# Kernel tuning notes

Measured on AMD Instinct MI355X. Metric: run time of the kernel, lower is better.

## Reference

```python
import jax, jax.numpy as jnp
import numpy as np

EPS = 1e-5
K = 3
N_TAP = K * K


def _bn(x, g, b, m, v):
    # eval-mode batchnorm over channel axis 1 of NCHW
    inv = g / jnp.sqrt(v + EPS)
    return x * inv[None, :, None, None] + (b - m * inv)[None, :, None, None]


def _silu(x):
    return x * jax.nn.sigmoid(x)


def _dcn(x, offset, mask, w, b, pad=1):
    """Modulated deformable conv (DCNv2), stride 1.
    x: [B,C,H,W], offset: [B,2n,H,W] ((dy,dx) per tap), mask: [B,n,H,W],
    w: [O,C,K,K], b: [O]."""
    B, C, H, W = x.shape
    O = w.shape[0]
    ky, kx = jnp.meshgrid(jnp.arange(K), jnp.arange(K), indexing='ij')
    ky = ky.reshape(N_TAP).astype(x.dtype)
    kx = kx.reshape(N_TAP).astype(x.dtype)
    off = offset.reshape(B, N_TAP, 2, H, W)
    base_y = jnp.arange(H, dtype=x.dtype)[None, None, :, None]
    base_x = jnp.arange(W, dtype=x.dtype)[None, None, None, :]
    # fractional sample positions [B,n,H,W]
    py = base_y - pad + ky[None, :, None, None] + off[:, :, 0]
    px = base_x - pad + kx[None, :, None, None] + off[:, :, 1]
    y0 = jnp.floor(py)
    x0 = jnp.floor(px)
    fy = py - y0
    fx = px - x0
    y0i = y0.astype(jnp.int32)
    x0i = x0.astype(jnp.int32)
    x_flat = x.reshape(B, C, 1, H * W)

    def corner(yi, xi, wgt):
        valid = (yi >= 0) & (yi < H) & (xi >= 0) & (xi < W)
        idx = (jnp.clip(yi, 0, H - 1) * W + jnp.clip(xi, 0, W - 1)).reshape(B, 1, N_TAP, H * W)
        v = jnp.take_along_axis(x_flat, idx, axis=-1)  # [B,C,n,HW]
        return v * (wgt * valid.astype(x.dtype)).reshape(B, 1, N_TAP, H * W)

    acc = corner(y0i, x0i, (1 - fy) * (1 - fx))
    acc = acc + corner(y0i, x0i + 1, (1 - fy) * fx)
    acc = acc + corner(y0i + 1, x0i, fy * (1 - fx))
    acc = acc + corner(y0i + 1, x0i + 1, fy * fx)
    val = acc.reshape(B, C, N_TAP, H, W) * mask[:, None]  # modulation
    out = jnp.einsum('bcnhw,ocn->bohw', val, w.reshape(O, C, N_TAP))
    return out + b[None, :, None, None]


def setup_inputs() -> dict:
    key = jax.random.key(0)
    ks = jax.random.split(key, 16)
    B, C1, H, W = 8, 256, 80, 80
    C2 = 256
    Ch = 128  # c_ = int(c2 * 0.5)
    d = {}
    d['x'] = jax.random.normal(ks[0], (B, C1, H, W), jnp.float32)
    # cv1: 1x1 conv (no bias) + BN
    d['cv1_w'] = jax.random.normal(ks[1], (Ch, C1), jnp.float32) * (1.0 / np.sqrt(C1))
    d['bn1_g'] = jax.random.uniform(ks[2], (Ch,), jnp.float32, 0.5, 1.5)
    d['bn1_b'] = jax.random.normal(ks[3], (Ch,), jnp.float32) * 0.1
    d['bn1_m'] = jax.random.normal(ks[4], (Ch,), jnp.float32) * 0.1
    d['bn1_v'] = jax.random.uniform(ks[5], (Ch,), jnp.float32, 0.5, 1.5)
    # offset/mask predictor 3x3 conv (small weights -> modest deformation)
    d['off_w'] = jax.random.normal(ks[6], (3 * N_TAP, Ch, K, K), jnp.float32) * 0.01
    d['off_b'] = jnp.zeros((3 * N_TAP,), jnp.float32)
    # dcn main weight/bias
    d['dcn_w'] = jax.random.normal(ks[7], (Ch, Ch, K, K), jnp.float32) * (1.0 / np.sqrt(Ch * N_TAP))
    d['dcn_b'] = jnp.zeros((Ch,), jnp.float32)
    d['bn2_g'] = jax.random.uniform(ks[8], (Ch,), jnp.float32, 0.5, 1.5)
    d['bn2_b'] = jax.random.normal(ks[9], (Ch,), jnp.float32) * 0.1
    d['bn2_m'] = jax.random.normal(ks[10], (Ch,), jnp.float32) * 0.1
    d['bn2_v'] = jax.random.uniform(ks[11], (Ch,), jnp.float32, 0.5, 1.5)
    # cv2: 1x1 conv (no bias) + BN
    d['cv2_w'] = jax.random.normal(ks[12], (C2, Ch), jnp.float32) * (1.0 / np.sqrt(Ch))
    d['bn3_g'] = jax.random.uniform(ks[13], (C2,), jnp.float32, 0.5, 1.5)
    d['bn3_b'] = jax.random.normal(ks[14], (C2,), jnp.float32) * 0.1
    d['bn3_m'] = jax.random.normal(ks[15], (C2,), jnp.float32) * 0.1
    d['bn3_v'] = jnp.ones((C2,), jnp.float32)
    return d


def reference(x, cv1_w, bn1_g, bn1_b, bn1_m, bn1_v,
              off_w, off_b, dcn_w, dcn_b, bn2_g, bn2_b, bn2_m, bn2_v,
              cv2_w, bn3_g, bn3_b, bn3_m, bn3_v):
    # cv1: 1x1 conv -> BN -> SiLU
    y = _silu(_bn(jnp.einsum('bchw,oc->bohw', x, cv1_w), bn1_g, bn1_b, bn1_m, bn1_v))
    # offset/mask predictor: 3x3 conv, pad 1
    raw = jax.lax.conv_general_dilated(
        y, off_w, window_strides=(1, 1), padding=((1, 1), (1, 1)),
        dimension_numbers=('NCHW', 'OIHW', 'NCHW')) + off_b[None, :, None, None]
    offset = raw[:, :2 * N_TAP]
    mask = jax.nn.sigmoid(raw[:, 2 * N_TAP:])
    # modulated deformable 3x3 conv -> BN -> SiLU
    y = _silu(_bn(_dcn(y, offset, mask, dcn_w, dcn_b), bn2_g, bn2_b, bn2_m, bn2_v))
    # cv2: 1x1 conv -> BN -> SiLU
    y = _silu(_bn(jnp.einsum('bchw,oc->bohw', y, cv2_w), bn3_g, bn3_b, bn3_m, bn3_v))
    return x + y  # shortcut (c1 == c2)
```

## Files before the change

kernel.cpp:

```cpp
#include <hip/hip_runtime.h>
#include <math.h>

#define HWSZ 6400
#define WIMG 80
#define HIMG 80
#define BEPS 1e-5f

typedef __attribute__((ext_vector_type(8))) short short8;
typedef __attribute__((ext_vector_type(4))) short s16x4;
typedef __attribute__((ext_vector_type(4))) float f32x4;

__device__ __forceinline__ unsigned short f2b(float f) {
    unsigned u = __builtin_bit_cast(unsigned, f);
    u += 0x7fffu + ((u >> 16) & 1u);
    return (unsigned short)(u >> 16);
}
__device__ __forceinline__ float b2f(unsigned short h) {
    unsigned u = ((unsigned)h) << 16;
    return __builtin_bit_cast(float, u);
}
__device__ __forceinline__ float silu_f(float t) { return t / (1.f + __expf(-t)); }

#define BPOS(sub, nt, n16, q) (((((sub)*4 + (nt))*16 + (n16))*40) + (q)*8)

__global__ __launch_bounds__(256) void k_prep(
    const float* __restrict__ cv1w, const float* __restrict__ g1, const float* __restrict__ b1,
    const float* __restrict__ m1, const float* __restrict__ v1,
    const float* __restrict__ offw, const float* __restrict__ offb,
    const float* __restrict__ dcnw, const float* __restrict__ dcnb,
    const float* __restrict__ g2, const float* __restrict__ b2,
    const float* __restrict__ m2, const float* __restrict__ v2,
    const float* __restrict__ cv2w, const float* __restrict__ g3, const float* __restrict__ b3,
    const float* __restrict__ m3, const float* __restrict__ v3,
    unsigned short* __restrict__ apk1, unsigned short* __restrict__ apko,
    unsigned short* __restrict__ apkd, unsigned short* __restrict__ apk2,
    float* __restrict__ bias1, float* __restrict__ biaso,
    float* __restrict__ bias2, float* __restrict__ bias3)
{
    int idx = blockIdx.x * 256 + threadIdx.x;
    if (idx < 32768) {
        int j = idx & 7, L = (idx >> 3) & 63, ks = (idx >> 9) & 7, mt = idx >> 12;
        int o = mt * 16 + (L & 15), k = ks * 32 + (L >> 4) * 8 + j;
        float inv = g1[o] * rsqrtf(v1[o] + BEPS);
        apk1[idx] = f2b(cv1w[o * 256 + k] * inv);
    } else if (idx < 69632) {
        int t = idx - 32768;
        int j = t & 7, L = (t >> 3) & 63;
        int mt = t / 18432, rem = t % 18432, ks = rem >> 9;
        int o = mt * 16 + (L & 15);
        int kp = ks * 32 + (L >> 4) * 8 + j;
        int n = kp >> 7, c = kp & 127;
        float wv = (o < 27) ? offw[(size_t)(o * 128 + c) * 9 + n] : 0.f;
        apko[t] = f2b(wv);
    } else if (idx < 217088) {
        int t = idx - 69632;
        int j = t & 7, L = (t >> 3) & 63;
        int mt = t / 18432, rem = t % 18432, ks = rem >> 9;
        int o = mt * 16 + (L & 15);
        int kp = ks * 32 + (L >> 4) * 8 + j;
        int n = kp >> 7, c = kp & 127;
        float inv = g2[o] * rsqrtf(v2[o] + BEPS);
        apkd[t] = f2b(dcnw[(size_t)(o * 128 + c) * 9 + n] * inv);
    } else if (idx < 249856) {
        int t = idx - 217088;
        int j = t & 7, L = (t >> 3) & 63, ks = (t >> 9) & 3, mt = t >> 11;
        int o = mt * 16 + (L & 15), k = ks * 32 + (L >> 4) * 8 + j;
        float inv = g3[o] * rsqrtf(v3[o] + BEPS);
        apk2[t] = f2b(cv2w[o * 128 + k] * inv);
    } else if (idx < 250395) {
        int t = idx - 249856;
        if (t < 128) { float inv = g1[t] * rsqrtf(v1[t] + BEPS); bias1[t] = b1[t] - m1[t] * inv; }
        else if (t < 155) { biaso[t - 128] = offb[t - 128]; }
        else if (t < 283) { int o = t - 155; float inv = g2[o] * rsqrtf(v2[o] + BEPS);
                            bias2[o] = dcnb[o] * inv + b2[o] - m2[o] * inv; }
        else { int o = t - 283; float inv = g3[o] * rsqrtf(v3[o] + BEPS); bias3[o] = b3[o] - m3[o] * inv; }
    }
}

__global__ __launch_bounds__(256) void k_cv1(
    const float* __restrict__ x, const unsigned short* __restrict__ apk1,
    const float* __restrict__ bias1, unsigned short* __restrict__ y1t)
{
    int blk = blockIdx.x;
    int b = blk & 7, pt = blk >> 3;
    int p0 = pt * 64;
    int tid = threadIdx.x;
    int lane = tid & 63, w = tid >> 6;
    int n16 = lane & 15, qd = lane >> 4;
    int px = p0 + w * 16 + n16;
    const float* xb = x + (size_t)b * 256 * HWSZ + px;
    f32x4 acc[8];
#pragma unroll
    for (int mt = 0; mt < 8; ++mt) acc[mt] = (f32x4){0.f, 0.f, 0.f, 0.f};
#pragma unroll 2
    for (int ks = 0; ks < 8; ++ks) {
        short8 bf;
#pragma unroll
        for (int j = 0; j < 8; ++j)
            bf[j] = (short)f2b(xb[(size_t)(ks * 32 + qd * 8 + j) * HWSZ]);
#pragma unroll
        for (int mt = 0; mt < 8; ++mt) {
            short8 af = *(const short8*)&apk1[(size_t)((mt * 8 + ks) * 64 + lane) * 8];
            acc[mt] = __builtin_amdgcn_mfma_f32_16x16x32_bf16(af, bf, acc[mt], 0, 0, 0);
        }
    }
    unsigned short* ytb = y1t + ((size_t)b * HWSZ + px) * 128;
#pragma unroll
    for (int mt = 0; mt < 8; ++mt) {
        int o0 = mt * 16 + qd * 4;
        s16x4 v;
#pragma unroll
        for (int r = 0; r < 4; ++r)
            v[r] = (short)f2b(silu_f(acc[mt][r] + bias1[o0 + r]));
        *(s16x4*)&ytb[o0] = v;
    }
}

__global__ __launch_bounds__(256) void k_off(
    const unsigned short* __restrict__ y1t, const unsigned short* __restrict__ apko,
    const float* __restrict__ biaso, float* __restrict__ raw)
{
    __shared__ __align__(16) unsigned short sV[10240];
    int blk = blockIdx.x;
    int b = blk & 7, pt = blk >> 3;
    int p0 = pt * 64;
    int tid = threadIdx.x;
    int lane = tid & 63, w = tid >> 6;
    int n16 = lane & 15, qd = lane >> 4;
    int pxl = tid >> 2, q = tid & 3;
    int p = p0 + pxl;
    int h = p / WIMG, wx = p % WIMG;
    const unsigned short* yb = y1t + (size_t)b * HWSZ * 128;
    f32x4 acc[2];
    acc[0] = (f32x4){0.f, 0.f, 0.f, 0.f};
    acc[1] = (f32x4){0.f, 0.f, 0.f, 0.f};
    const short8 zz = {0, 0, 0, 0, 0, 0, 0, 0};
    for (int n = 0; n < 9; ++n) {
        int hh = h - 1 + n / 3, ww = wx - 1 + n % 3;
        bool valid = ((unsigned)hh < HIMG) && ((unsigned)ww < WIMG);
        int spx = valid ? hh * WIMG + ww : 0;
        const unsigned short* ys = yb + (size_t)spx * 128 + q * 8;
#pragma unroll
        for (int sub = 0; sub < 4; ++sub) {
            short8 v = *(const short8*)&ys[sub * 32];
            if (!valid) v = zz;
            *(short8*)&sV[BPOS(sub, pxl >> 4, pxl & 15, q)] = v;
        }
        __syncthreads();
#pragma unroll
        for (int sub = 0; sub < 4; ++sub) {
            int ks = n * 4 + sub;
            short8 bf = *(const short8*)&sV[BPOS(sub, w, n16, qd)];
#pragma unroll
            for (int mi = 0; mi < 2; ++mi) {
                short8 af = *(const short8*)&apko[(size_t)((mi * 36 + ks) * 64 + lane) * 8];
                acc[mi] = __builtin_amdgcn_mfma_f32_16x16x32_bf16(af, bf, acc[mi], 0, 0, 0);
            }
        }
        __syncthreads();
    }
    float* rb = raw + (size_t)b * 27 * HWSZ + p0 + w * 16 + n16;
#pragma unroll
    for (int mi = 0; mi < 2; ++mi)
#pragma unroll
        for (int r = 0; r < 4; ++r) {
            int o = mi * 16 + qd * 4 + r;
            if (o < 27) {
                float t = acc[mi][r] + biaso[o];
                if (o >= 18) t = 1.f / (1.f + __expf(-t));
                rb[(size_t)o * HWSZ] = t;
            }
        }
}

__global__ __launch_bounds__(256) void k_dcn(
    const unsigned short* __restrict__ y1t, const float* __restrict__ raw,
    const unsigned short* __restrict__ apkd, const float* __restrict__ bias2,
    unsigned short* __restrict__ zt)
{
    __shared__ float swgt[4][9][64];
    __shared__ unsigned short sidx[4][9][64];
    __shared__ __align__(16) unsigned short sV[10240];
    int blk = blockIdx.x;
    int b = blk & 7, pt = blk >> 3;
    int p0 = pt * 64;
    int tid = threadIdx.x;

    for (int i = tid; i < 576; i += 256) {
        int n = i / 64, pp = i % 64;
        int p = p0 + pp;
        int h = p / WIMG, wx = p % WIMG;
        const float* rb = raw + (size_t)b * 27 * HWSZ + p;
        float dy = rb[(size_t)(2 * n) * HWSZ];
        float dx = rb[(size_t)(2 * n + 1) * HWSZ];
        float mk = rb[(size_t)(18 + n) * HWSZ];
        float py = (float)(h - 1 + n / 3) + dy;
        float px = (float)(wx - 1 + n % 3) + dx;
        float y0f = floorf(py), x0f = floorf(px);
        float fy = py - y0f, fx = px - x0f;
        int y0 = (int)y0f, x0 = (int)x0f;
#pragma unroll
        for (int k = 0; k < 4; ++k) {
            int yy = y0 + (k >> 1);
            int xx = x0 + (k & 1);
            bool valid = ((unsigned)yy < HIMG) && ((unsigned)xx < WIMG);
            float wk = ((k >> 1) ? fy : 1.f - fy) * ((k & 1) ? fx : 1.f - fx);
            wk = valid ? wk * mk : 0.f;
            int yc = min(max(yy, 0), HIMG - 1);
            int xc = min(max(xx, 0), WIMG - 1);
            sidx[k][n][pp] = (unsigned short)(yc * WIMG + xc);
            swgt[k][n][pp] = wk;
        }
    }
    __syncthreads();

    int lane = tid & 63, w = tid >> 6;
    int n16 = lane & 15, qd = lane >> 4;
    int pxl = tid >> 2, q = tid & 3;
    const unsigned short* yb = y1t + (size_t)b * HWSZ * 128;
    f32x4 acc[2][4];
#pragma unroll
    for (int mi = 0; mi < 2; ++mi)
#pragma unroll
        for (int nt = 0; nt < 4; ++nt) acc[mi][nt] = (f32x4){0.f, 0.f, 0.f, 0.f};

    for (int n = 0; n < 9; ++n) {
        float av[4][8];
#pragma unroll
        for (int sub = 0; sub < 4; ++sub)
#pragma unroll
            for (int j = 0; j < 8; ++j) av[sub][j] = 0.f;
#pragma unroll
        for (int k = 0; k < 4; ++k) {
            float wk = swgt[k][n][pxl];
            const unsigned short* ys = yb + (size_t)sidx[k][n][pxl] * 128 + q * 8;
#pragma unroll
            for (int sub = 0; sub < 4; ++sub) {
                short8 v = *(const short8*)&ys[sub * 32];
#pragma unroll
                for (int j = 0; j < 8; ++j)
                    av[sub][j] = fmaf(wk, b2f((unsigned short)v[j]), av[sub][j]);
            }
        }
#pragma unroll
        for (int sub = 0; sub < 4; ++sub) {
            short8 v;
#pragma unroll
            for (int j = 0; j < 8; ++j) v[j] = (short)f2b(av[sub][j]);
            *(short8*)&sV[BPOS(sub, pxl >> 4, pxl & 15, q)] = v;
        }
        __syncthreads();
#pragma unroll
        for (int sub = 0; sub < 4; ++sub) {
            int ks = n * 4 + sub;
            short8 bf[4];
#pragma unroll
            for (int nt = 0; nt < 4; ++nt)
                bf[nt] = *(const short8*)&sV[BPOS(sub, nt, n16, qd)];
#pragma unroll
            for (int mi = 0; mi < 2; ++mi) {
                short8 af = *(const short8*)&apkd[(size_t)(((2 * w + mi) * 36 + ks) * 64 + lane) * 8];
#pragma unroll
                for (int nt = 0; nt < 4; ++nt)
                    acc[mi][nt] = __builtin_amdgcn_mfma_f32_16x16x32_bf16(af, bf[nt], acc[mi][nt], 0, 0, 0);
            }
        }
        __syncthreads();
    }
    unsigned short* zb = zt + ((size_t)b * HWSZ + p0) * 128;
#pragma unroll
    for (int mi = 0; mi < 2; ++mi)
#pragma unroll
        for (int nt = 0; nt < 4; ++nt) {
            int o0 = (2 * w + mi) * 16 + qd * 4;
            int px = nt * 16 + n16;
            s16x4 v;
#pragma unroll
            for (int r = 0; r < 4; ++r)
                v[r] = (short)f2b(silu_f(acc[mi][nt][r] + bias2[o0 + r]));
            *(s16x4*)&zb[(size_t)px * 128 + o0] = v;
        }
}

__global__ __launch_bounds__(256) void k_cv2(
    const unsigned short* __restrict__ zt, const float* __restrict__ x,
    const unsigned short* __restrict__ apk2, const float* __restrict__ bias3,
    float* __restrict__ out)
{
    int blk = blockIdx.x;
    int b = blk & 7, pt = blk >> 3;
    int p0 = pt * 64;
    int tid = threadIdx.x;
    int lane = tid & 63, w = tid >> 6;
    int n16 = lane & 15, qd = lane >> 4;
    const unsigned short* zb = zt + ((size_t)b * HWSZ + p0) * 128;
    f32x4 acc[4][4];
#pragma unroll
    for (int mi = 0; mi < 4; ++mi)
#pragma unroll
        for (int nt = 0; nt < 4; ++nt) acc[mi][nt] = (f32x4){0.f, 0.f, 0.f, 0.f};
#pragma unroll
    for (int ks = 0; ks < 4; ++ks) {
        short8 bf[4];
#pragma unroll
        for (int nt = 0; nt < 4; ++nt)
            bf[nt] = *(const short8*)&zb[(size_t)(nt * 16 + n16) * 128 + ks * 32 + qd * 8];
#pragma unroll
        for (int mi = 0; mi < 4; ++mi) {
            int mt = w * 4 + mi;
            short8 af = *(const short8*)&apk2[(size_t)((mt * 4 + ks) * 64 + lane) * 8];
#pragma unroll
            for (int nt = 0; nt < 4; ++nt)
                acc[mi][nt] = __builtin_amdgcn_mfma_f32_16x16x32_bf16(af, bf[nt], acc[mi][nt], 0, 0, 0);
        }
    }
    const float* xb = x + (size_t)b * 256 * HWSZ;
    float* ob = out + (size_t)b * 256 * HWSZ;
#pragma unroll
    for (int mi = 0; mi < 4; ++mi)
#pragma unroll
        for (int nt = 0; nt < 4; ++nt)
#pragma unroll
            for (int r = 0; r < 4; ++r) {
                int o = w * 64 + mi * 16 + qd * 4 + r;
                size_t idx = (size_t)o * HWSZ + p0 + nt * 16 + n16;
                ob[idx] = xb[idx] + silu_f(acc[mi][nt][r] + bias3[o]);
            }
}

extern "C" void kernel_launch(void* const* d_in, const int* in_sizes, int n_in,
                              void* d_out, int out_size, void* d_ws, size_t ws_size,
                              hipStream_t stream) {
    const float* x     = (const float*)d_in[0];
    const float* cv1w  = (const float*)d_in[1];
    const float* bn1g  = (const float*)d_in[2];
    const float* bn1b  = (const float*)d_in[3];
    const float* bn1m  = (const float*)d_in[4];
    const float* bn1v  = (const float*)d_in[5];
    const float* offw  = (const float*)d_in[6];
    const float* offb  = (const float*)d_in[7];
    const float* dcnw  = (const float*)d_in[8];
    const float* dcnb  = (const float*)d_in[9];
    const float* bn2g  = (const float*)d_in[10];
    const float* bn2b  = (const float*)d_in[11];
    const float* bn2m  = (const float*)d_in[12];
    const float* bn2v  = (const float*)d_in[13];
    const float* cv2w  = (const float*)d_in[14];
    const float* bn3g  = (const float*)d_in[15];
    const float* bn3b  = (const float*)d_in[16];
    const float* bn3m  = (const float*)d_in[17];
    const float* bn3v  = (const float*)d_in[18];
    float* out = (float*)d_out;

    float* base = (float*)d_ws;
    unsigned short* y1t = (unsigned short*)base;
    float* raw   = base + 3276800;
    unsigned short* zt  = (unsigned short*)(base + 4659200);
    unsigned short* apk1 = (unsigned short*)(base + 7936000);
    unsigned short* apko = (unsigned short*)(base + 7952384);
    unsigned short* apkd = (unsigned short*)(base + 7970816);
    unsigned short* apk2 = (unsigned short*)(base + 8044544);
    float* bias1 = base + 8060928;
    float* biaso = base + 8061056;
    float* bias2 = base + 8061088;
    float* bias3 = base + 8061216;

    k_prep<<<979, 256, 0, stream>>>(cv1w, bn1g, bn1b, bn1m, bn1v,
                                    offw, offb, dcnw, dcnb,
                                    bn2g, bn2b, bn2m, bn2v,
                                    cv2w, bn3g, bn3b, bn3m, bn3v,
                                    apk1, apko, apkd, apk2,
                                    bias1, biaso, bias2, bias3);
    k_cv1<<<800, 256, 0, stream>>>(x, apk1, bias1, y1t);
    k_off<<<800, 256, 0, stream>>>(y1t, apko, biaso, raw);
    k_dcn<<<800, 256, 0, stream>>>(y1t, raw, apkd, bias2, zt);
    k_cv2<<<800, 256, 0, stream>>>(zt, x, apk2, bias3, out);
}
```

Measured before the change: 260.3 us.

## Vectorize epilogue stores, drop LDS staging in offset conv, pack bf16 conversions

```diff
diff --git a/kernel.cpp b/kernel.cpp
--- a/kernel.cpp
+++ b/kernel.cpp
@@ -9,11 +9,19 @@
 typedef __attribute__((ext_vector_type(8))) short short8;
 typedef __attribute__((ext_vector_type(4))) short s16x4;
 typedef __attribute__((ext_vector_type(4))) float f32x4;
+typedef __attribute__((ext_vector_type(4))) int i32x4;
 
 __device__ __forceinline__ unsigned short f2b(float f) {
     unsigned u = __builtin_bit_cast(unsigned, f);
     u += 0x7fffu + ((u >> 16) & 1u);
     return (unsigned short)(u >> 16);
+}
+__device__ __forceinline__ int f2b_pk(float flo, float fhi) {
+    unsigned lo = __builtin_bit_cast(unsigned, flo);
+    unsigned hi = __builtin_bit_cast(unsigned, fhi);
+    lo += 0x7fffu + ((lo >> 16) & 1u);
+    hi += 0x7fffu + ((hi >> 16) & 1u);
+    return (int)__builtin_amdgcn_perm(hi, lo, 0x07060302u);
 }
 __device__ __forceinline__ float b2f(unsigned short h) {
     unsigned u = ((unsigned)h) << 16;
@@ -92,12 +100,16 @@
     f32x4 acc[8];
 #pragma unroll
     for (int mt = 0; mt < 8; ++mt) acc[mt] = (f32x4){0.f, 0.f, 0.f, 0.f};
-#pragma unroll 2
+#pragma unroll
     for (int ks = 0; ks < 8; ++ks) {
-        short8 bf;
+        float xv[8];
 #pragma unroll
         for (int j = 0; j < 8; ++j)
-            bf[j] = (short)f2b(xb[(size_t)(ks * 32 + qd * 8 + j) * HWSZ]);
+            xv[j] = xb[(size_t)(ks * 32 + qd * 8 + j) * HWSZ];
+        i32x4 bi;
+#pragma unroll
+        for (int t = 0; t < 4; ++t) bi[t] = f2b_pk(xv[2 * t], xv[2 * t + 1]);
+        short8 bf = __builtin_bit_cast(short8, bi);
 #pragma unroll
         for (int mt = 0; mt < 8; ++mt) {
             short8 af = *(const short8*)&apk1[(size_t)((mt * 8 + ks) * 64 + lane) * 8];
@@ -120,44 +132,40 @@
     const unsigned short* __restrict__ y1t, const unsigned short* __restrict__ apko,
     const float* __restrict__ biaso, float* __restrict__ raw)
 {
-    __shared__ __align__(16) unsigned short sV[10240];
     int blk = blockIdx.x;
     int b = blk & 7, pt = blk >> 3;
     int p0 = pt * 64;
     int tid = threadIdx.x;
     int lane = tid & 63, w = tid >> 6;
     int n16 = lane & 15, qd = lane >> 4;
-    int pxl = tid >> 2, q = tid & 3;
+    int pxl = w * 16 + n16;
     int p = p0 + pxl;
     int h = p / WIMG, wx = p % WIMG;
-    const unsigned short* yb = y1t + (size_t)b * HWSZ * 128;
+    const unsigned short* yb = y1t + (size_t)b * HWSZ * 128 + qd * 8;
     f32x4 acc[2];
     acc[0] = (f32x4){0.f, 0.f, 0.f, 0.f};
     acc[1] = (f32x4){0.f, 0.f, 0.f, 0.f};
     const short8 zz = {0, 0, 0, 0, 0, 0, 0, 0};
+#pragma unroll
     for (int n = 0; n < 9; ++n) {
         int hh = h - 1 + n / 3, ww = wx - 1 + n % 3;
         bool valid = ((unsigned)hh < HIMG) && ((unsigned)ww < WIMG);
         int spx = valid ? hh * WIMG + ww : 0;
-        const unsigned short* ys = yb + (size_t)spx * 128 + q * 8;
+        const unsigned short* ys = yb + (size_t)spx * 128;
+        short8 v[4];
 #pragma unroll
         for (int sub = 0; sub < 4; ++sub) {
-            short8 v = *(const short8*)&ys[sub * 32];
-            if (!valid) v = zz;
-            *(short8*)&sV[BPOS(sub, pxl >> 4, pxl & 15, q)] = v;
-        }
-        __syncthreads();
+            v[sub] = *(const short8*)&ys[sub * 32];
+            if (!valid) v[sub] = zz;
+        }
 #pragma unroll
         for (int sub = 0; sub < 4; ++sub) {
             int ks = n * 4 + sub;
-            short8 bf = *(const short8*)&sV[BPOS(sub, w, n16, qd)];
-#pragma unroll
-            for (int mi = 0; mi < 2; ++mi) {
-                short8 af = *(const short8*)&apko[(size_t)((mi * 36 + ks) * 64 + lane) * 8];
-                acc[mi] = __builtin_amdgcn_mfma_f32_16x16x32_bf16(af, bf, acc[mi], 0, 0, 0);
-            }
-        }
-        __syncthreads();
+            short8 af0 = *(const short8*)&apko[(size_t)(ks * 64 + lane) * 8];
+            short8 af1 = *(const short8*)&apko[(size_t)((36 + ks) * 64 + lane) * 8];
+            acc[0] = __builtin_amdgcn_mfma_f32_16x16x32_bf16(af0, v[sub], acc[0], 0, 0, 0);
+            acc[1] = __builtin_amdgcn_mfma_f32_16x16x32_bf16(af1, v[sub], acc[1], 0, 0, 0);
+        }
     }
     float* rb = raw + (size_t)b * 27 * HWSZ + p0 + w * 16 + n16;
 #pragma unroll
@@ -244,10 +252,11 @@
         }
 #pragma unroll
         for (int sub = 0; sub < 4; ++sub) {
-            short8 v;
-#pragma unroll
-            for (int j = 0; j < 8; ++j) v[j] = (short)f2b(av[sub][j]);
-            *(short8*)&sV[BPOS(sub, pxl >> 4, pxl & 15, q)] = v;
+            i32x4 bi;
+#pragma unroll
+            for (int t = 0; t < 4; ++t)
+                bi[t] = f2b_pk(av[sub][2 * t], av[sub][2 * t + 1]);
+            *(i32x4*)&sV[BPOS(sub, pxl >> 4, pxl & 15, q)] = bi;
         }
         __syncthreads();
 #pragma unroll
@@ -296,36 +305,43 @@
     const unsigned short* zb = zt + ((size_t)b * HWSZ + p0) * 128;
     f32x4 acc[4][4];
 #pragma unroll
-    for (int mi = 0; mi < 4; ++mi)
-#pragma unroll
-        for (int nt = 0; nt < 4; ++nt) acc[mi][nt] = (f32x4){0.f, 0.f, 0.f, 0.f};
+    for (int mt = 0; mt < 4; ++mt)
+#pragma unroll
+        for (int ntl = 0; ntl < 4; ++ntl) acc[mt][ntl] = (f32x4){0.f, 0.f, 0.f, 0.f};
 #pragma unroll
     for (int ks = 0; ks < 4; ++ks) {
-        short8 bf[4];
-#pragma unroll
-        for (int nt = 0; nt < 4; ++nt)
-            bf[nt] = *(const short8*)&zb[(size_t)(nt * 16 + n16) * 128 + ks * 32 + qd * 8];
-#pragma unroll
-        for (int mi = 0; mi < 4; ++mi) {
-            int mt = w * 4 + mi;
-            short8 af = *(const short8*)&apk2[(size_t)((mt * 4 + ks) * 64 + lane) * 8];
-#pragma unroll
-            for (int nt = 0; nt < 4; ++nt)
-                acc[mi][nt] = __builtin_amdgcn_mfma_f32_16x16x32_bf16(af, bf[nt], acc[mi][nt], 0, 0, 0);
+        short8 az[4];
+#pragma unroll
+        for (int mt = 0; mt < 4; ++mt)
+            az[mt] = *(const short8*)&zb[(size_t)(mt * 16 + n16) * 128 + ks * 32 + qd * 8];
+#pragma unroll
+        for (int ntl = 0; ntl < 4; ++ntl) {
+            int nt = w * 4 + ntl;
+            short8 bw = *(const short8*)&apk2[(size_t)((nt * 4 + ks) * 64 + lane) * 8];
+#pragma unroll
+            for (int mt = 0; mt < 4; ++mt)
+                acc[mt][ntl] = __builtin_amdgcn_mfma_f32_16x16x32_bf16(az[mt], bw, acc[mt][ntl], 0, 0, 0);
         }
     }
     const float* xb = x + (size_t)b * 256 * HWSZ;
     float* ob = out + (size_t)b * 256 * HWSZ;
 #pragma unroll
-    for (int mi = 0; mi < 4; ++mi)
-#pragma unroll
-        for (int nt = 0; nt < 4; ++nt)
-#pragma unroll
-            for (int r = 0; r < 4; ++r) {
-                int o = w * 64 + mi * 16 + qd * 4 + r;
-                size_t idx = (size_t)o * HWSZ + p0 + nt * 16 + n16;
-                ob[idx] = xb[idx] + silu_f(acc[mi][nt][r] + bias3[o]);
-            }
+    for (int mt = 0; mt < 4; ++mt) {
+        int px = p0 + mt * 16 + qd * 4;
+#pragma unroll
+        for (int ntl = 0; ntl < 4; ++ntl) {
+            int o = (w * 4 + ntl) * 16 + n16;
+            float bv = bias3[o];
+            size_t base = (size_t)o * HWSZ + px;
+            float4 xv = *(const float4*)&xb[base];
+            float4 r;
+            r.x = xv.x + silu_f(acc[mt][ntl][0] + bv);
+            r.y = xv.y + silu_f(acc[mt][ntl][1] + bv);
+            r.z = xv.z + silu_f(acc[mt][ntl][2] + bv);
+            r.w = xv.w + silu_f(acc[mt][ntl][3] + bv);
+            *(float4*)&ob[base] = r;
+        }
+    }
 }
 
 extern "C" void kernel_launch(void* const* d_in, const int* in_sizes, int n_in,
```

Measured after the change: 262.2 us. About the same (+0.7%).
